# Kernel tuning notes

Hardware: AMD Instinct MI355X
Metric: run time of the kernel (lower is better)

The kernel has to match this reference:

```python
import jax, jax.numpy as jnp
import numpy as np

B, C_IN, C_OUT, K, H, W_DIM, F_IN = 16, 64, 64, 3, 128, 128, 16
NKW = C_OUT * C_IN * K * K  # 36864 kernel weights per sample


def setup_inputs() -> dict:
    key = jax.random.key(0)
    ks = jax.random.split(key, 8)
    s = 0.05
    return {
        "x": jax.random.normal(ks[0], (B, C_IN, H, W_DIM), dtype=jnp.float32),
        "z": jax.random.normal(ks[1], (B, F_IN), dtype=jnp.float32),
        "W0": jax.random.normal(ks[2], (20, F_IN), dtype=jnp.float32) * s,
        "b0": jax.random.normal(ks[3], (20,), dtype=jnp.float32) * s,
        "W1": jax.random.normal(ks[4], (30, 20), dtype=jnp.float32) * s,
        "b1": jax.random.normal(ks[5], (30,), dtype=jnp.float32) * s,
        "W2": jax.random.normal(ks[6], (NKW + C_OUT, 30), dtype=jnp.float32) * s,
        "b2": jax.random.normal(ks[7], (NKW + C_OUT,), dtype=jnp.float32) * s,
    }


def reference(x, z, W0, b0, W1, b1, W2, b2):
    # Manifold MLP: ReLU after EVERY layer, including the final one (as in original code).
    h = jax.nn.relu(z @ W0.T + b0)
    h = jax.nn.relu(h @ W1.T + b1)
    aw = jax.nn.relu(h @ W2.T + b2)  # [B, NKW + C_OUT]

    kernels = aw[:, :NKW].reshape(B, C_OUT, C_IN, K, K)  # per-sample OIHW kernels
    biases = aw[:, NKW:]  # [B, C_OUT]

    def conv_one(xi, wi, bi):
        # xi: [C_IN, H, W], wi: [C_OUT, C_IN, K, K], bi: [C_OUT]
        y = jax.lax.conv_general_dilated(
            xi[None], wi, window_strides=(1, 1), padding="SAME",
            dimension_numbers=("NCHW", "OIHW", "NCHW"))[0]
        return y + bi[:, None, None]

    out = jax.vmap(conv_one)(x, kernels, biases)  # [B, C_OUT, H, W]
    return jax.nn.relu(out)
```

## Files before the change

kernel.cpp:

```cpp
#include <hip/hip_runtime.h>


typedef __bf16 bf16;
typedef __bf16 bf16x8 __attribute__((ext_vector_type(8)));
typedef float f32x4 __attribute__((ext_vector_type(4)));

#define NB 16
#define CI 64
#define CO 64
#define HH 128
#define WW 128
#define TS 16
#define HALO 18
#define CPAD 72
#define WPAD 72
#define NKW 36864
#define NROWS 36928

__global__ __launch_bounds__(256)
void hyper_kernel(const float* __restrict__ z, const float* __restrict__ W0,
                  const float* __restrict__ b0, const float* __restrict__ W1,
                  const float* __restrict__ b1, const float* __restrict__ W2,
                  const float* __restrict__ b2, bf16* __restrict__ wt,
                  float* __restrict__ biases) {
  __shared__ float h1s[NB][30];
  const int tid = threadIdx.x;
  if (tid < NB) {
    float h0[20];
    #pragma unroll
    for (int i = 0; i < 20; ++i) {
      float s = b0[i];
      #pragma unroll
      for (int j = 0; j < 16; ++j) s += W0[i * 16 + j] * z[tid * 16 + j];
      h0[i] = fmaxf(s, 0.f);
    }
    #pragma unroll
    for (int i = 0; i < 30; ++i) {
      float s = b1[i];
      #pragma unroll
      for (int j = 0; j < 20; ++j) s += W1[i * 20 + j] * h0[j];
      h1s[tid][i] = fmaxf(s, 0.f);
    }
  }
  __syncthreads();
  const int r = blockIdx.x * 256 + tid;
  if (r >= NROWS) return;
  float w2r[30];
  #pragma unroll
  for (int j = 0; j < 30; ++j) w2r[j] = W2[r * 30 + j];
  const float bb = b2[r];
  const bool isk = r < NKW;
  int co = 0, ci = 0, tap = 0;
  if (isk) {
    co = r / 576;
    int rem = r - co * 576;
    ci = rem / 9;
    tap = rem - ci * 9;
  }
  for (int b = 0; b < NB; ++b) {
    float s = bb;
    #pragma unroll
    for (int j = 0; j < 30; ++j) s += w2r[j] * h1s[b][j];
    s = fmaxf(s, 0.f);
    if (isk)
      wt[((size_t)((b * 9 + tap) * CO + co)) * CI + ci] = (bf16)s;
    else
      biases[b * CO + (r - NKW)] = s;
  }
}

__global__ __launch_bounds__(1024)
void conv_kernel(const float* __restrict__ x, const bf16* __restrict__ wt,
                 const float* __restrict__ bias, float* __restrict__ out) {
  __shared__ __align__(16) bf16 xt[HALO * HALO * CPAD];
  __shared__ __align__(16) bf16 wts[CO * WPAD];

  const int b = blockIdx.z;
  const int x0 = blockIdx.x * TS;
  const int y0 = blockIdx.y * TS;
  const int tid = threadIdx.x;

  for (int e = tid; e < HALO * HALO * CI; e += 1024) {
    int ci = e / (HALO * HALO);
    int p = e - ci * (HALO * HALO);
    int py = p / HALO;
    int px = p - py * HALO;
    int gy = y0 + py - 1, gx = x0 + px - 1;
    float v = 0.f;
    if (gy >= 0 && gy < HH && gx >= 0 && gx < WW)
      v = x[((size_t)(b * CI + ci) * HH + gy) * WW + gx];
    xt[(py * HALO + px) * CPAD + ci] = (bf16)v;
  }

  const int lane = tid & 63;
  const int wv = tid >> 6;
  const int m = lane & 15;
  const int q = lane >> 4;
  const int cg0 = (wv & 1) * 2;
  const int ty0 = (wv >> 1) * 2;

  f32x4 acc[2][2];
  #pragma unroll
  for (int i = 0; i < 2; ++i)
    #pragma unroll
    for (int j = 0; j < 2; ++j) acc[i][j] = (f32x4){0.f, 0.f, 0.f, 0.f};

  const int wco = tid >> 4;
  const int wci = (tid & 15) * 4;
  const bf16* wsrc = wt + (size_t)b * 9 * CO * CI + (size_t)wco * CI + wci;

  for (int tap = 0; tap < 9; ++tap) {
    __syncthreads();
    *reinterpret_cast<uint2*>(&wts[wco * WPAD + wci]) =
        *reinterpret_cast<const uint2*>(wsrc + (size_t)tap * CO * CI);
    __syncthreads();
    const int dy = tap / 3, dx = tap - dy * 3;
    #pragma unroll
    for (int kh = 0; kh < 2; ++kh) {
      const int ci0 = kh * 32 + q * 8;
      bf16x8 a0 = *reinterpret_cast<const bf16x8*>(
          &wts[(cg0 * 16 + m) * WPAD + ci0]);
      bf16x8 a1 = *reinterpret_cast<const bf16x8*>(
          &wts[((cg0 + 1) * 16 + m) * WPAD + ci0]);
      bf16x8 bv0 = *reinterpret_cast<const bf16x8*>(
          &xt[((ty0 + dy) * HALO + (m + dx)) * CPAD + ci0]);
      bf16x8 bv1 = *reinterpret_cast<const bf16x8*>(
          &xt[((ty0 + 1 + dy) * HALO + (m + dx)) * CPAD + ci0]);
      acc[0][0] = __builtin_amdgcn_mfma_f32_16x16x32_bf16(a0, bv0, acc[0][0], 0, 0, 0);
      acc[0][1] = __builtin_amdgcn_mfma_f32_16x16x32_bf16(a0, bv1, acc[0][1], 0, 0, 0);
      acc[1][0] = __builtin_amdgcn_mfma_f32_16x16x32_bf16(a1, bv0, acc[1][0], 0, 0, 0);
      acc[1][1] = __builtin_amdgcn_mfma_f32_16x16x32_bf16(a1, bv1, acc[1][1], 0, 0, 0);
    }
  }

  #pragma unroll
  for (int i = 0; i < 2; ++i) {
    #pragma unroll
    for (int j = 0; j < 2; ++j) {
      const int gy = y0 + ty0 + j;
      #pragma unroll
      for (int r = 0; r < 4; ++r) {
        const int co = (cg0 + i) * 16 + q * 4 + r;
        float v = acc[i][j][r] + bias[b * CO + co];
        out[((size_t)(b * CO + co) * HH + gy) * WW + x0 + m] = fmaxf(v, 0.f);
      }
    }
  }
}

extern "C" void kernel_launch(void* const* d_in, const int* in_sizes, int n_in,
                              void* d_out, int out_size, void* d_ws,
                              size_t ws_size, hipStream_t stream) {
  const float* x = (const float*)d_in[0];
  const float* z = (const float*)d_in[1];
  const float* W0 = (const float*)d_in[2];
  const float* b0 = (const float*)d_in[3];
  const float* W1 = (const float*)d_in[4];
  const float* b1 = (const float*)d_in[5];
  const float* W2 = (const float*)d_in[6];
  const float* b2 = (const float*)d_in[7];
  float* out = (float*)d_out;

  bf16* wt = (bf16*)d_ws;
  float* biases = (float*)((char*)d_ws + (size_t)NB * 9 * CO * CI * 2);

  hipLaunchKernelGGL(hyper_kernel, dim3((NROWS + 255) / 256), dim3(256), 0,
                     stream, z, W0, b0, W1, b1, W2, b2, wt, biases);
  hipLaunchKernelGGL(conv_kernel, dim3(WW / TS, HH / TS, NB), dim3(1024), 0,
                     stream, x, wt, biases, out);
}
```

Baseline: 184.8 us.

## Pre-swizzle weights into MFMA fragment layout and load directly from global

The hyper kernel now writes generated weights in a layout matching the MFMA A-fragment order, so the conv kernel loads each lane's fragments straight from global memory and no longer stages weights in LDS with two barriers per tap. The input halo tile drops its padding, uses an XOR swizzle against bank conflicts, and is loaded eight channels at a time as packed bf16x8 stores. Blocks shrink to 512 threads, each wave covering all 64 output channels for two rows, with setprio around the MFMA section. The cost is more registers for weight fragments and repeated global or L2 weight reads across waves.

```diff
diff --git a/kernel.cpp b/kernel.cpp
--- a/kernel.cpp
+++ b/kernel.cpp
@@ -12,16 +12,16 @@
 #define WW 128
 #define TS 16
 #define HALO 18
-#define CPAD 72
-#define WPAD 72
+#define NPL (HALO * HALO)
 #define NKW 36864
 #define NROWS 36928
+#define WT2_BYTES ((size_t)NB * 9 * 4096 * 2)
 
 __global__ __launch_bounds__(256)
 void hyper_kernel(const float* __restrict__ z, const float* __restrict__ W0,
                   const float* __restrict__ b0, const float* __restrict__ W1,
                   const float* __restrict__ b1, const float* __restrict__ W2,
-                  const float* __restrict__ b2, bf16* __restrict__ wt,
+                  const float* __restrict__ b2, bf16* __restrict__ wt2,
                   float* __restrict__ biases) {
   __shared__ float h1s[NB][30];
   const int tid = threadIdx.x;
@@ -50,12 +50,15 @@
   for (int j = 0; j < 30; ++j) w2r[j] = W2[r * 30 + j];
   const float bb = b2[r];
   const bool isk = r < NKW;
-  int co = 0, ci = 0, tap = 0;
+  size_t base = 0;
   if (isk) {
-    co = r / 576;
-    int rem = r - co * 576;
-    ci = rem / 9;
-    tap = rem - ci * 9;
+    const int co = r / 576;
+    const int rem = r - co * 576;
+    const int ci = rem / 9;
+    const int tap = rem - ci * 9;
+    const int g = co >> 4, mm = co & 15;
+    const int kh = ci >> 5, qq = (ci >> 3) & 3, jj = ci & 7;
+    base = (size_t)(tap * 8 + g * 2 + kh) * 512 + (size_t)(qq * 16 + mm) * 8 + jj;
   }
   for (int b = 0; b < NB; ++b) {
     float s = bb;
@@ -63,89 +66,100 @@
     for (int j = 0; j < 30; ++j) s += w2r[j] * h1s[b][j];
     s = fmaxf(s, 0.f);
     if (isk)
-      wt[((size_t)((b * 9 + tap) * CO + co)) * CI + ci] = (bf16)s;
+      wt2[(size_t)b * (9 * 4096) + base] = (bf16)s;
     else
       biases[b * CO + (r - NKW)] = s;
   }
 }
 
-__global__ __launch_bounds__(1024)
-void conv_kernel(const float* __restrict__ x, const bf16* __restrict__ wt,
+__global__ __launch_bounds__(512, 4)
+void conv_kernel(const float* __restrict__ x, const bf16* __restrict__ wt2,
                  const float* __restrict__ bias, float* __restrict__ out) {
-  __shared__ __align__(16) bf16 xt[HALO * HALO * CPAD];
-  __shared__ __align__(16) bf16 wts[CO * WPAD];
+  __shared__ __align__(16) bf16 xt[NPL * 64];
 
   const int b = blockIdx.z;
   const int x0 = blockIdx.x * TS;
   const int y0 = blockIdx.y * TS;
   const int tid = threadIdx.x;
-
-  for (int e = tid; e < HALO * HALO * CI; e += 1024) {
-    int ci = e / (HALO * HALO);
-    int p = e - ci * (HALO * HALO);
-    int py = p / HALO;
-    int px = p - py * HALO;
-    int gy = y0 + py - 1, gx = x0 + px - 1;
-    float v = 0.f;
-    if (gy >= 0 && gy < HH && gx >= 0 && gx < WW)
-      v = x[((size_t)(b * CI + ci) * HH + gy) * WW + gx];
-    xt[(py * HALO + px) * CPAD + ci] = (bf16)v;
-  }
-
   const int lane = tid & 63;
   const int wv = tid >> 6;
   const int m = lane & 15;
   const int q = lane >> 4;
-  const int cg0 = (wv & 1) * 2;
-  const int ty0 = (wv >> 1) * 2;
 
-  f32x4 acc[2][2];
+  for (int it = tid; it < NPL * 8; it += 512) {
+    const int pl = it >> 3, cig = it & 7;
+    const int py = (pl * 57) >> 10;
+    const int px = pl - py * 18;
+    const int gy = y0 + py - 1, gx = x0 + px - 1;
+    const bool inb = ((unsigned)gy < (unsigned)HH) & ((unsigned)gx < (unsigned)WW);
+    bf16x8 v8;
+    #pragma unroll
+    for (int j = 0; j < 8; ++j) v8[j] = (bf16)0.f;
+    if (inb) {
+      const float* src =
+          x + ((size_t)(b * CI + cig * 8) << 14) + (size_t)(gy * WW + gx);
+      #pragma unroll
+      for (int j = 0; j < 8; ++j) v8[j] = (bf16)src[(size_t)j << 14];
+    }
+    *reinterpret_cast<bf16x8*>(reinterpret_cast<char*>(xt) + (pl << 7) +
+                               ((cig ^ (pl & 7)) << 4)) = v8;
+  }
+
+  f32x4 acc[4][2];
   #pragma unroll
-  for (int i = 0; i < 2; ++i)
+  for (int i = 0; i < 4; ++i) {
+    acc[i][0] = (f32x4){0.f, 0.f, 0.f, 0.f};
+    acc[i][1] = (f32x4){0.f, 0.f, 0.f, 0.f};
+  }
+
+  const char* wbase = (const char*)wt2 + (size_t)b * (9 * 8192) + lane * 16;
+  const int ty0 = wv * 2;
+
+  __syncthreads();
+
+  #pragma unroll 1
+  for (int tap = 0; tap < 9; ++tap) {
+    const char* wt_tap = wbase + tap * 8192;
+    bf16x8 a[4][2];
     #pragma unroll
-    for (int j = 0; j < 2; ++j) acc[i][j] = (f32x4){0.f, 0.f, 0.f, 0.f};
-
-  const int wco = tid >> 4;
-  const int wci = (tid & 15) * 4;
-  const bf16* wsrc = wt + (size_t)b * 9 * CO * CI + (size_t)wco * CI + wci;
-
-  for (int tap = 0; tap < 9; ++tap) {
-    __syncthreads();
-    *reinterpret_cast<uint2*>(&wts[wco * WPAD + wci]) =
-        *reinterpret_cast<const uint2*>(wsrc + (size_t)tap * CO * CI);
-    __syncthreads();
-    const int dy = tap / 3, dx = tap - dy * 3;
+    for (int i = 0; i < 4; ++i)
+      #pragma unroll
+      for (int kh = 0; kh < 2; ++kh)
+        a[i][kh] = *reinterpret_cast<const bf16x8*>(wt_tap + (i * 2 + kh) * 1024);
+    const int dy = (tap * 11) >> 5;
+    const int dx = tap - dy * 3;
+    const int plb = (ty0 + dy) * 18 + dx + m;
+    __builtin_amdgcn_s_setprio(1);
     #pragma unroll
     for (int kh = 0; kh < 2; ++kh) {
-      const int ci0 = kh * 32 + q * 8;
-      bf16x8 a0 = *reinterpret_cast<const bf16x8*>(
-          &wts[(cg0 * 16 + m) * WPAD + ci0]);
-      bf16x8 a1 = *reinterpret_cast<const bf16x8*>(
-          &wts[((cg0 + 1) * 16 + m) * WPAD + ci0]);
-      bf16x8 bv0 = *reinterpret_cast<const bf16x8*>(
-          &xt[((ty0 + dy) * HALO + (m + dx)) * CPAD + ci0]);
-      bf16x8 bv1 = *reinterpret_cast<const bf16x8*>(
-          &xt[((ty0 + 1 + dy) * HALO + (m + dx)) * CPAD + ci0]);
-      acc[0][0] = __builtin_amdgcn_mfma_f32_16x16x32_bf16(a0, bv0, acc[0][0], 0, 0, 0);
-      acc[0][1] = __builtin_amdgcn_mfma_f32_16x16x32_bf16(a0, bv1, acc[0][1], 0, 0, 0);
-      acc[1][0] = __builtin_amdgcn_mfma_f32_16x16x32_bf16(a1, bv0, acc[1][0], 0, 0, 0);
-      acc[1][1] = __builtin_amdgcn_mfma_f32_16x16x32_bf16(a1, bv1, acc[1][1], 0, 0, 0);
+      const int qk = q + kh * 4;
+      #pragma unroll
+      for (int j = 0; j < 2; ++j) {
+        const int pl = plb + j * 18;
+        const bf16x8 bv = *reinterpret_cast<const bf16x8*>(
+            reinterpret_cast<const char*>(xt) + (pl << 7) +
+            ((qk ^ (pl & 7)) << 4));
+        #pragma unroll
+        for (int i = 0; i < 4; ++i)
+          acc[i][j] =
+              __builtin_amdgcn_mfma_f32_16x16x32_bf16(a[i][kh], bv, acc[i][j], 0, 0, 0);
+      }
     }
+    __builtin_amdgcn_s_setprio(0);
   }
 
+  const float* bp = bias + b * CO;
+  float* ob = out + ((size_t)(b * CO) << 14) + (size_t)((y0 + ty0) * WW + x0 + m);
   #pragma unroll
-  for (int i = 0; i < 2; ++i) {
+  for (int i = 0; i < 4; ++i)
     #pragma unroll
-    for (int j = 0; j < 2; ++j) {
-      const int gy = y0 + ty0 + j;
+    for (int j = 0; j < 2; ++j)
       #pragma unroll
       for (int r = 0; r < 4; ++r) {
-        const int co = (cg0 + i) * 16 + q * 4 + r;
-        float v = acc[i][j][r] + bias[b * CO + co];
-        out[((size_t)(b * CO + co) * HH + gy) * WW + x0 + m] = fmaxf(v, 0.f);
+        const int co = i * 16 + q * 4 + r;
+        float v = acc[i][j][r] + bp[co];
+        ob[((size_t)co << 14) + j * WW] = fmaxf(v, 0.f);
       }
-    }
-  }
 }
 
 extern "C" void kernel_launch(void* const* d_in, const int* in_sizes, int n_in,
@@ -161,11 +175,11 @@
   const float* b2 = (const float*)d_in[7];
   float* out = (float*)d_out;
 
-  bf16* wt = (bf16*)d_ws;
-  float* biases = (float*)((char*)d_ws + (size_t)NB * 9 * CO * CI * 2);
+  bf16* wt2 = (bf16*)d_ws;
+  float* biases = (float*)((char*)d_ws + WT2_BYTES);
 
   hipLaunchKernelGGL(hyper_kernel, dim3((NROWS + 255) / 256), dim3(256), 0,
-                     stream, z, W0, b0, W1, b1, W2, b2, wt, biases);
-  hipLaunchKernelGGL(conv_kernel, dim3(WW / TS, HH / TS, NB), dim3(1024), 0,
-                     stream, x, wt, biases, out);
+                     stream, z, W0, b0, W1, b1, W2, b2, wt2, biases);
+  hipLaunchKernelGGL(conv_kernel, dim3(WW / TS, HH / TS, NB), dim3(512), 0,
+                     stream, x, wt2, biases, out);
 }
```

Measured after the change: 191.9 us. 3.8% more time.
